# Performance work log

Measured on AMD Instinct MI355X. Metric: run time of the kernel, lower is better.

The kernel has to match this reference:

```python
import jax, jax.numpy as jnp
import numpy as np

B, S, D, H = 2, 2048, 1024, 16
DK = D // H

def setup_inputs() -> dict:
    key = jax.random.key(0)
    ks = jax.random.split(key, 8)
    scale = 1.0 / np.sqrt(D)
    return {
        "q": jax.random.normal(ks[0], (B, S, D), jnp.float32),
        "k": jax.random.normal(ks[1], (B, S, D), jnp.float32),
        "v": jax.random.normal(ks[2], (B, S, D), jnp.float32),
        "reaches": jax.random.uniform(ks[3], (B, S), jnp.float32),
        "Wq": jax.random.normal(ks[4], (D, D), jnp.float32) * scale,
        "Wk": jax.random.normal(ks[5], (D, D), jnp.float32) * scale,
        "Wv": jax.random.normal(ks[6], (D, D), jnp.float32) * scale,
        "Wo": jax.random.normal(ks[7], (D, D), jnp.float32) * scale,
    }

def _split_heads(x):
    # [B,S,D] -> [B,H,S,DK]
    return x.reshape(B, S, H, DK).transpose(0, 2, 1, 3)

def reference(q, k, v, reaches, Wq, Wk, Wv, Wo):
    # torch Linear: y = x @ W.T
    qh = _split_heads(q @ Wq.T)
    kh = _split_heads(k @ Wk.T)
    vh = _split_heads(v @ Wv.T)
    scores = jnp.einsum("bhqd,bhkd->bhqk", qh, kh) / jnp.sqrt(jnp.float32(DK))
    scores = jax.nn.softmax(scores, axis=-1)
    # post-softmax reach weighting along key axis
    scores = scores * reaches[:, None, None, :]
    # diagonal suppression: scores - scores*0.999999*eye
    scores = scores * (1.0 - 0.999999 * jnp.eye(S, dtype=scores.dtype))
    # inverted combine
    out = vh - jnp.einsum("bhqk,bhkd->bhqd", scores, vh)
    # per-position contribution rescale
    rs = reaches.sum(axis=-1, keepdims=True)
    contrib = (rs - reaches) / (rs + 1e-9) * (1.0 - reaches) * 100.0  # [B,S]
    out = out * contrib[:, None, :, None]
    concat = out.transpose(0, 2, 1, 3).reshape(B, S, D)
    return concat @ Wo.T
```

## Files before the change

kernel.cpp:

```cpp
#include <hip/hip_runtime.h>
#include <hip/hip_bf16.h>

typedef __attribute__((ext_vector_type(8))) short short8;
typedef __attribute__((ext_vector_type(4))) float f32x4;
typedef __attribute__((ext_vector_type(16))) float f32x16;
typedef unsigned short us;

#define B_ 2
#define S_ 2048
#define D_ 1024
#define H_ 16
#define DK_ 64
#define QSCALE 0.1803368867f

__device__ __forceinline__ us f2bf(float f) {
  union { float f; unsigned u; } x; x.f = f;
  unsigned r = x.u + 0x7FFFu + ((x.u >> 16) & 1u);
  return (us)(r >> 16);
}
__device__ __forceinline__ float bf2f(us h) {
  union { unsigned u; float f; } x; x.u = ((unsigned)h) << 16;
  return x.f;
}
__device__ __forceinline__ us f2bf_hw(float f) {
  __hip_bfloat16 h = __float2bfloat16(f);
  return *reinterpret_cast<us*>(&h);
}
__device__ __forceinline__ unsigned cvtpk(float lo, float hi) {
  unsigned r;
  asm("v_cvt_pk_bf16_f32 %0, %1, %2" : "=v"(r) : "v"(lo), "v"(hi));
  return r;
}

__device__ __forceinline__ void gload16(const void* g, void* l) {
  __builtin_amdgcn_global_load_lds((const __attribute__((address_space(1))) void*)g,
                                   (__attribute__((address_space(3))) void*)l, 16, 0, 0);
}

__global__ __launch_bounds__(256) void cvt_all(const float* __restrict__ q,
                                               const float* __restrict__ k,
                                               const float* __restrict__ v,
                                               const float* __restrict__ Wq,
                                               const float* __restrict__ Wk,
                                               const float* __restrict__ Wv,
                                               const float* __restrict__ Wo,
                                               us* __restrict__ oq, us* __restrict__ ok,
                                               us* __restrict__ ov, us* __restrict__ oWq,
                                               us* __restrict__ oWk, us* __restrict__ oWv,
                                               us* __restrict__ oWo) {
  int bid = blockIdx.x;
  const float* in; us* out; int off;
  if (bid < 12288) {
    int t = bid >> 12;
    in = (t == 0) ? q : (t == 1) ? k : v;
    out = (t == 0) ? oq : (t == 1) ? ok : ov;
    off = (bid & 4095) * 1024;
  } else {
    int t = (bid - 12288) >> 10;
    in = (t == 0) ? Wq : (t == 1) ? Wk : (t == 2) ? Wv : Wo;
    out = (t == 0) ? oWq : (t == 1) ? oWk : (t == 2) ? oWv : oWo;
    off = ((bid - 12288) & 1023) * 1024;
  }
  int i = off + threadIdx.x * 4;
  float4 val = *reinterpret_cast<const float4*>(in + i);
  ushort4 o;
  o.x = f2bf(val.x); o.y = f2bf(val.y); o.z = f2bf(val.z); o.w = f2bf(val.w);
  *reinterpret_cast<ushort4*>(out + i) = o;
}

__global__ __launch_bounds__(256) void rs_kernel(const float* __restrict__ reaches,
                                                 float* __restrict__ rs) {
  int b = blockIdx.x, t = threadIdx.x;
  float s = 0.f;
  for (int i = t; i < S_; i += 256) s += reaches[b * S_ + i];
  for (int o = 32; o > 0; o >>= 1) s += __shfl_down(s, o, 64);
  __shared__ float tmp[4];
  if ((t & 63) == 0) tmp[t >> 6] = s;
  __syncthreads();
  if (t == 0) rs[b] = tmp[0] + tmp[1] + tmp[2] + tmp[3];
}

__device__ __forceinline__ void gemm_core_hs(const us* __restrict__ A, const us* __restrict__ Bt,
                                             us* __restrict__ outH, float oscale) {
  __shared__ __align__(16) us lA[3][128 * 32];
  __shared__ __align__(16) us lB[3][128 * 32];
  const int tid = threadIdx.x;
  const int bm = blockIdx.x >> 3, bn = blockIdx.x & 7;
  const int w = tid >> 6, lane = tid & 63;
  const int wr = (w >> 1) * 64, wc = (w & 1) * 64;
  const int lr = lane & 15, lg = lane >> 4;

  f32x4 acc[4][4];
#pragma unroll
  for (int i = 0; i < 4; ++i)
#pragma unroll
    for (int j = 0; j < 4; ++j) acc[i][j] = (f32x4){0.f, 0.f, 0.f, 0.f};

  const int crow = lane >> 2, ce8 = (lane & 3) * 8;
  const us* A0 = A + (size_t)(bm * 128 + w * 32 + crow) * 1024 + ce8;
  const us* A1 = A0 + (size_t)16 * 1024;
  const us* B0 = Bt + (size_t)(bn * 128 + w * 32 + crow) * 1024 + ce8;
  const us* B1 = B0 + (size_t)16 * 1024;
  const int dA0 = (w * 32) * 32, dA1 = (w * 32 + 16) * 32;

  gload16(A0, &lA[0][dA0]);
  gload16(A1, &lA[0][dA1]);
  gload16(B0, &lB[0][dA0]);
  gload16(B1, &lB[0][dA1]);

  int cur = 0, nxt = 1;
  for (int kt = 0; kt < 32; ++kt) {
    if (kt < 31) {
      int ko = (kt + 1) * 32;
      gload16(A0 + ko, &lA[nxt][dA0]);
      gload16(A1 + ko, &lA[nxt][dA1]);
      gload16(B0 + ko, &lB[nxt][dA0]);
      gload16(B1 + ko, &lB[nxt][dA1]);
      asm volatile("s_waitcnt vmcnt(4)" ::: "memory");
    } else {
      asm volatile("s_waitcnt vmcnt(0)" ::: "memory");
    }
    __builtin_amdgcn_s_barrier();
    __builtin_amdgcn_sched_barrier(0);

    short8 af[4], bfr[4];
#pragma unroll
    for (int i = 0; i < 4; ++i)
      af[i] = *reinterpret_cast<const short8*>(&lA[cur][(wr + i * 16 + lr) * 32 + lg * 8]);
#pragma unroll
    for (int j = 0; j < 4; ++j)
      bfr[j] = *reinterpret_cast<const short8*>(&lB[cur][(wc + j * 16 + lr) * 32 + lg * 8]);
    __builtin_amdgcn_s_setprio(1);
#pragma unroll
    for (int i = 0; i < 4; ++i)
#pragma unroll
      for (int j = 0; j < 4; ++j)
        acc[i][j] = __builtin_amdgcn_mfma_f32_16x16x32_bf16(af[i], bfr[j], acc[i][j], 0, 0, 0);
    __builtin_amdgcn_s_setprio(0);

    cur = nxt;
    nxt = (nxt == 2) ? 0 : nxt + 1;
  }
#pragma unroll
  for (int i = 0; i < 4; ++i)
#pragma unroll
    for (int j = 0; j < 4; ++j)
#pragma unroll
      for (int ii = 0; ii < 4; ++ii) {
        int r = bm * 128 + wr + i * 16 + lg * 4 + ii;
        int c = bn * 128 + wc + j * 16 + lr;
        float v = acc[i][j][ii] * oscale;
        int b = r >> 11, s = r & (S_ - 1), h = c >> 6, dk = c & 63;
        outH[(((size_t)(b * H_ + h) * S_ + s) * DK_) + dk] = f2bf(v);
      }
}

__global__ __launch_bounds__(256) void proj_gemm(const us* __restrict__ q_bf,
                                                 const us* __restrict__ k_bf,
                                                 const us* __restrict__ v_bf,
                                                 const us* __restrict__ Wq_bf,
                                                 const us* __restrict__ Wk_bf,
                                                 const us* __restrict__ Wv_bf,
                                                 us* __restrict__ Qh, us* __restrict__ Kh,
                                                 us* __restrict__ Vh) {
  if (blockIdx.y == 0) gemm_core_hs(q_bf, Wq_bf, Qh, QSCALE);
  else if (blockIdx.y == 1) gemm_core_hs(k_bf, Wk_bf, Kh, 1.0f);
  else gemm_core_hs(v_bf, Wv_bf, Vh, 1.0f);
}

__global__ __launch_bounds__(256) void wo_gemm(const us* __restrict__ A,
                                               const us* __restrict__ Bt,
                                               float* __restrict__ outF) {
  __shared__ __align__(16) us lA[3][128 * 32];
  __shared__ __align__(16) us lB[3][64 * 32];
  const int tid = threadIdx.x;
  const int bm = blockIdx.x >> 4, bn = blockIdx.x & 15;
  const int w = tid >> 6, lane = tid & 63;
  const int lr = lane & 15, lg = lane >> 4;

  f32x4 acc[2][4];
#pragma unroll
  for (int i = 0; i < 2; ++i)
#pragma unroll
    for (int j = 0; j < 4; ++j) acc[i][j] = (f32x4){0.f, 0.f, 0.f, 0.f};

  const int crow = lane >> 2, ce8 = (lane & 3) * 8;
  const us* A0 = A + (size_t)(bm * 128 + w * 32 + crow) * 1024 + ce8;
  const us* A1 = A0 + (size_t)16 * 1024;
  const us* B0 = Bt + (size_t)(bn * 64 + w * 16 + crow) * 1024 + ce8;
  const int dA0 = (w * 32) * 32, dA1 = (w * 32 + 16) * 32, dB0 = (w * 16) * 32;

  gload16(A0, &lA[0][dA0]);
  gload16(A1, &lA[0][dA1]);
  gload16(B0, &lB[0][dB0]);

  int cur = 0, nxt = 1;
  for (int kt = 0; kt < 32; ++kt) {
    if (kt < 31) {
      int ko = (kt + 1) * 32;
      gload16(A0 + ko, &lA[nxt][dA0]);
      gload16(A1 + ko, &lA[nxt][dA1]);
      gload16(B0 + ko, &lB[nxt][dB0]);
      asm volatile("s_waitcnt vmcnt(3)" ::: "memory");
    } else {
      asm volatile("s_waitcnt vmcnt(0)" ::: "memory");
    }
    __builtin_amdgcn_s_barrier();
    __builtin_amdgcn_sched_barrier(0);

    short8 af[2], bfr[4];
#pragma unroll
    for (int i = 0; i < 2; ++i)
      af[i] = *reinterpret_cast<const short8*>(&lA[cur][(w * 32 + i * 16 + lr) * 32 + lg * 8]);
#pragma unroll
    for (int j = 0; j < 4; ++j)
      bfr[j] = *reinterpret_cast<const short8*>(&lB[cur][(j * 16 + lr) * 32 + lg * 8]);
    __builtin_amdgcn_s_setprio(1);
#pragma unroll
    for (int i = 0; i < 2; ++i)
#pragma unroll
      for (int j = 0; j < 4; ++j)
        acc[i][j] = __builtin_amdgcn_mfma_f32_16x16x32_bf16(af[i], bfr[j], acc[i][j], 0, 0, 0);
    __builtin_amdgcn_s_setprio(0);

    cur = nxt;
    nxt = (nxt == 2) ? 0 : nxt + 1;
  }
#pragma unroll
  for (int i = 0; i < 2; ++i)
#pragma unroll
    for (int j = 0; j < 4; ++j)
#pragma unroll
      for (int ii = 0; ii < 4; ++ii) {
        int r = bm * 128 + w * 32 + i * 16 + lg * 4 + ii;
        int c = bn * 64 + j * 16 + lr;
        outF[(size_t)r * 1024 + c] = acc[i][j][ii];
      }
}

__global__ __launch_bounds__(256) void transp_kernel(const us* __restrict__ Vh,
                                                     const float* __restrict__ reaches,
                                                     us* __restrict__ VhTw) {
  __shared__ us t[64 * 68];
  const int bh = blockIdx.x >> 5, st = blockIdx.x & 31;
  const int b = bh >> 4;
  const size_t base = (size_t)bh * S_ * DK_;
  const int r = threadIdx.x >> 3, e8 = (threadIdx.x & 7) * 8;
#pragma unroll
  for (int h2 = 0; h2 < 2; ++h2) {
    int row = r + h2 * 32;
    *reinterpret_cast<short8*>(&t[row * 68 + e8]) =
        *reinterpret_cast<const short8*>(&Vh[base + (size_t)(st * 64 + row) * DK_ + e8]);
  }
  __syncthreads();
#pragma unroll
  for (int h2 = 0; h2 < 2; ++h2) {
    int dk = (threadIdx.x >> 3) + h2 * 32;
    int sc = (threadIdx.x & 7) * 8;
    short8 v;
#pragma unroll
    for (int j = 0; j < 8; ++j) {
      float rw = reaches[b * S_ + st * 64 + sc + j];
      v[j] = (short)f2bf_hw(bf2f(t[(sc + j) * 68 + dk]) * rw);
    }
    *reinterpret_cast<short8*>(&VhTw[base + (size_t)dk * S_ + st * 64 + sc]) = v;
  }
}

__global__ __launch_bounds__(256, 2) void attn_kernel(const us* __restrict__ Qh,
                                                      const us* __restrict__ Kh,
                                                      const us* __restrict__ Vh,
                                                      const us* __restrict__ VhTw,
                                                      const float* __restrict__ reaches,
                                                      const float* __restrict__ rsum,
                                                      us* __restrict__ concat) {
  __shared__ __align__(16) us sbuf[3][8192];
  __shared__ float diagP[128];
  __shared__ float lsum[128];

  const int tid = threadIdx.x;
  const int bid = ((blockIdx.x & 7) << 6) | (blockIdx.x >> 3);
  const int qt = bid & 15;
  const int bh = bid >> 4;
  const int b = bh >> 4, h = bh & 15;
  const size_t base = (size_t)bh * S_ * DK_;

  const int w = tid >> 6, lane = tid & 63;
  const int l31 = lane & 31, hh = lane >> 5, l7 = lane & 7;
  const int h4 = hh * 4;
  const int diagkt = qt * 2 + (w >> 1);

  const int Lrow = lane >> 3;
  const int cswz = (l7 ^ Lrow) << 3;
  const us* Kg0 = Kh + base + (size_t)(w * 16 + Lrow) * DK_ + cswz;
  const us* Kg1 = Kg0 + (size_t)8 * DK_;
  const us* Vg0 = VhTw + base + (size_t)(w * 16 + Lrow) * S_ + cswz;
  const us* Vg1 = Vg0 + (size_t)8 * S_;
  const int dK0 = (w * 16) * 64, dK1 = (w * 16 + 8) * 64;
  const int dV0 = 4096 + dK0, dV1 = 4096 + dK1;

  short8 aq[4];
  {
    const us* qp = &Qh[base + (size_t)(qt * 128 + w * 32 + l31) * DK_ + hh * 8];
#pragma unroll
    for (int dk = 0; dk < 4; ++dk)
      aq[dk] = *reinterpret_cast<const short8*>(qp + dk * 16);
  }

  int rdK[2][4];
#pragma unroll
  for (int c = 0; c < 2; ++c)
#pragma unroll
    for (int dk = 0; dk < 4; ++dk)
      rdK[c][dk] = (c * 32 + l31) * 64 + (((dk * 2 + hh) ^ l7) << 3);

  gload16(Kg0, &sbuf[0][dK0]);
  gload16(Kg1, &sbuf[0][dK1]);
  gload16(Vg0, &sbuf[0][dV0]);
  gload16(Vg1, &sbuf[0][dV1]);

  f32x16 oacc[2];
  float lacc = 0.f;
#pragma unroll
  for (int c = 0; c < 2; ++c)
#pragma unroll
    for (int r = 0; r < 16; ++r) oacc[c][r] = 0.f;

  int cur = 0, nxt = 1;
  for (int kt = 0; kt < 32; ++kt) {
    if (kt < 31) {
      const size_t ko = (size_t)(kt + 1) * 64;
      gload16(Kg0 + ko * DK_, &sbuf[nxt][dK0]);
      gload16(Kg1 + ko * DK_, &sbuf[nxt][dK1]);
      gload16(Vg0 + ko, &sbuf[nxt][dV0]);
      gload16(Vg1 + ko, &sbuf[nxt][dV1]);
      asm volatile("s_waitcnt vmcnt(4)" ::: "memory");
    } else {
      asm volatile("s_waitcnt vmcnt(0)" ::: "memory");
    }
    __builtin_amdgcn_s_barrier();
    __builtin_amdgcn_sched_barrier(0);

    const us* lKc = &sbuf[cur][0];
    const us* vTc = &sbuf[cur][4096];

    f32x16 st0, st1;
#pragma unroll
    for (int r = 0; r < 16; ++r) { st0[r] = 0.f; st1[r] = 0.f; }
    __builtin_amdgcn_s_setprio(1);
#pragma unroll
    for (int dk = 0; dk < 4; ++dk) {
      short8 k0 = *reinterpret_cast<const short8*>(&lKc[rdK[0][dk]]);
      st0 = __builtin_amdgcn_mfma_f32_32x32x16_bf16(k0, aq[dk], st0, 0, 0, 0);
      short8 k1 = *reinterpret_cast<const short8*>(&lKc[rdK[1][dk]]);
      st1 = __builtin_amdgcn_mfma_f32_32x32x16_bf16(k1, aq[dk], st1, 0, 0, 0);
    }
    __builtin_amdgcn_s_setprio(0);

    float e0[16], e1[16];
#pragma unroll
    for (int r = 0; r < 16; ++r) {
      e0[r] = __builtin_amdgcn_exp2f(st0[r]);
      e1[r] = __builtin_amdgcn_exp2f(st1[r]);
      lacc += e0[r] + e1[r];
    }
    if (kt == diagkt) {
#pragma unroll
      for (int r = 0; r < 16; ++r) {
        int kk = (r & 3) + 8 * (r >> 2) + 4 * hh;
        float ev = (w & 1) ? e1[r] : e0[r];
        if (kk == l31) diagP[w * 32 + l31] = ev;
      }
    }

    short8 pa[4];
#pragma unroll
    for (int ks = 0; ks < 4; ++ks) {
      const int ro = (ks & 1) * 8;
      unsigned d0, s0, d1, s1;
      if (ks < 2) {
        d0 = cvtpk(e0[ro + 0], e0[ro + 1]);
        s0 = cvtpk(e0[ro + 4], e0[ro + 5]);
        d1 = cvtpk(e0[ro + 2], e0[ro + 3]);
        s1 = cvtpk(e0[ro + 6], e0[ro + 7]);
      } else {
        d0 = cvtpk(e1[ro + 0], e1[ro + 1]);
        s0 = cvtpk(e1[ro + 4], e1[ro + 5]);
        d1 = cvtpk(e1[ro + 2], e1[ro + 3]);
        s1 = cvtpk(e1[ro + 6], e1[ro + 7]);
      }
      asm("v_permlane32_swap_b32 %0, %1" : "+v"(d0), "+v"(s0));
      asm("v_permlane32_swap_b32 %0, %1" : "+v"(d1), "+v"(s1));
      union { unsigned u[4]; short8 v; } pk;
      pk.u[0] = d0; pk.u[1] = d1; pk.u[2] = s0; pk.u[3] = s1;
      pa[ks] = pk.v;
    }

    __builtin_amdgcn_s_setprio(1);
#pragma unroll
    for (int dc = 0; dc < 2; ++dc)
#pragma unroll
      for (int ks = 0; ks < 4; ++ks) {
        short8 bv = *reinterpret_cast<const short8*>(&vTc[rdK[dc][ks]]);
        oacc[dc] = __builtin_amdgcn_mfma_f32_32x32x16_bf16(pa[ks], bv, oacc[dc], 0, 0, 0);
      }
    __builtin_amdgcn_s_setprio(0);

    cur = nxt;
    nxt = (nxt == 2) ? 0 : nxt + 1;
  }

  lacc += __shfl_xor(lacc, 32, 64);
  if (hh == 0) lsum[w * 32 + l31] = lacc;
  __syncthreads();

  const float rb = rsum[b];
#pragma unroll
  for (int r = 0; r < 16; ++r) {
    const int q = w * 32 + (r & 3) + 8 * (r >> 2) + h4;
    const int qg = qt * 128 + q;
    const float rq = reaches[b * S_ + qg];
    const float contrib = (rb - rq) / (rb + 1e-9f) * (1.f - rq) * 100.f;
    const float corr = 0.999999f * diagP[q] * rq;
    const float linv = 1.0f / lsum[q];
#pragma unroll
    for (int dc = 0; dc < 2; ++dc) {
      int d = dc * 32 + l31;
      float vhv = bf2f(Vh[base + (size_t)qg * DK_ + d]);
      float pv = (oacc[dc][r] - corr * vhv) * linv;
      float o = (vhv - pv) * contrib;
      concat[((size_t)(b * S_ + qg)) * D_ + h * 64 + d] = f2bf(o);
    }
  }
}

extern "C" void kernel_launch(void* const* d_in, const int* in_sizes, int n_in,
                              void* d_out, int out_size, void* d_ws, size_t ws_size,
                              hipStream_t stream) {
  const float* q = (const float*)d_in[0];
  const float* k = (const float*)d_in[1];
  const float* v = (const float*)d_in[2];
  const float* reaches = (const float*)d_in[3];
  const float* Wq = (const float*)d_in[4];
  const float* Wk = (const float*)d_in[5];
  const float* Wv = (const float*)d_in[6];
  const float* Wo = (const float*)d_in[7];

  const size_t NQKV = (size_t)B_ * S_ * D_;
  const size_t NW = (size_t)D_ * D_;

  us* q_bf = (us*)d_ws;
  us* k_bf = q_bf + NQKV;
  us* v_bf = k_bf + NQKV;
  us* Wq_bf = v_bf + NQKV;
  us* Wk_bf = Wq_bf + NW;
  us* Wv_bf = Wk_bf + NW;
  us* Wo_bf = Wv_bf + NW;
  us* Qh = Wo_bf + NW;
  us* Kh = Qh + NQKV;
  us* Vh = Kh + NQKV;
  us* concat = Vh + NQKV;
  float* rs = (float*)(concat + NQKV);
  us* VhTw = q_bf;

  cvt_all<<<16384, 256, 0, stream>>>(q, k, v, Wq, Wk, Wv, Wo,
                                     q_bf, k_bf, v_bf, Wq_bf, Wk_bf, Wv_bf, Wo_bf);
  rs_kernel<<<B_, 256, 0, stream>>>(reaches, rs);

  proj_gemm<<<dim3(256, 3), 256, 0, stream>>>(q_bf, k_bf, v_bf, Wq_bf, Wk_bf, Wv_bf, Qh, Kh, Vh);
  transp_kernel<<<B_ * H_ * (S_ / 64), 256, 0, stream>>>(Vh, reaches, VhTw);

  attn_kernel<<<B_ * H_ * (S_ / 128), 256, 0, stream>>>(Qh, Kh, Vh, VhTw, reaches, rs, concat);

  wo_gemm<<<512, 256, 0, stream>>>(concat, Wo_bf, (float*)d_out);
}
```

Before: 133.2 us.

## Fold reach-sum into conversion kernel, swizzle GEMM tiles, register-staged attention loads

The reach-sum reduction now runs in one extra block of the conversion kernel, which removes a separate launch. The projection and output GEMMs remap block indices so that neighbouring blocks share operand tiles, aiming for better L2 reuse. The attention kernel replaces its triple-buffered direct global-to-LDS loads with register prefetch into a double-buffered LDS array, with a full block barrier each iteration. That change cuts LDS use, which may raise occupancy, but it adds register pressure and extra synchronisation, and global latency may be less well hidden.

After: 127.2 us (median of 3 runs). 1.05x faster.

```diff
diff --git a/kernel.cpp b/kernel.cpp
--- a/kernel.cpp
+++ b/kernel.cpp
@@ -44,11 +44,26 @@
                                                const float* __restrict__ Wk,
                                                const float* __restrict__ Wv,
                                                const float* __restrict__ Wo,
+                                               const float* __restrict__ reaches,
                                                us* __restrict__ oq, us* __restrict__ ok,
                                                us* __restrict__ ov, us* __restrict__ oWq,
                                                us* __restrict__ oWk, us* __restrict__ oWv,
-                                               us* __restrict__ oWo) {
+                                               us* __restrict__ oWo, float* __restrict__ rs) {
   int bid = blockIdx.x;
+  if (bid >= 16384) {
+    __shared__ float tmp[4];
+    int t = threadIdx.x;
+    for (int b = 0; b < B_; ++b) {
+      float s = 0.f;
+      for (int i = t; i < S_; i += 256) s += reaches[b * S_ + i];
+      for (int o = 32; o > 0; o >>= 1) s += __shfl_down(s, o, 64);
+      if ((t & 63) == 0) tmp[t >> 6] = s;
+      __syncthreads();
+      if (t == 0) rs[b] = tmp[0] + tmp[1] + tmp[2] + tmp[3];
+      __syncthreads();
+    }
+    return;
+  }
   const float* in; us* out; int off;
   if (bid < 12288) {
     int t = bid >> 12;
@@ -68,24 +83,13 @@
   *reinterpret_cast<ushort4*>(out + i) = o;
 }
 
-__global__ __launch_bounds__(256) void rs_kernel(const float* __restrict__ reaches,
-                                                 float* __restrict__ rs) {
-  int b = blockIdx.x, t = threadIdx.x;
-  float s = 0.f;
-  for (int i = t; i < S_; i += 256) s += reaches[b * S_ + i];
-  for (int o = 32; o > 0; o >>= 1) s += __shfl_down(s, o, 64);
-  __shared__ float tmp[4];
-  if ((t & 63) == 0) tmp[t >> 6] = s;
-  __syncthreads();
-  if (t == 0) rs[b] = tmp[0] + tmp[1] + tmp[2] + tmp[3];
-}
-
 __device__ __forceinline__ void gemm_core_hs(const us* __restrict__ A, const us* __restrict__ Bt,
                                              us* __restrict__ outH, float oscale) {
   __shared__ __align__(16) us lA[3][128 * 32];
   __shared__ __align__(16) us lB[3][128 * 32];
   const int tid = threadIdx.x;
-  const int bm = blockIdx.x >> 3, bn = blockIdx.x & 7;
+  const int swz = (blockIdx.x & 7) * 32 + (blockIdx.x >> 3);
+  const int bm = swz >> 3, bn = swz & 7;
   const int w = tid >> 6, lane = tid & 63;
   const int wr = (w >> 1) * 64, wc = (w & 1) * 64;
   const int lr = lane & 15, lg = lane >> 4;
@@ -174,7 +178,8 @@
   __shared__ __align__(16) us lA[3][128 * 32];
   __shared__ __align__(16) us lB[3][64 * 32];
   const int tid = threadIdx.x;
-  const int bm = blockIdx.x >> 4, bn = blockIdx.x & 15;
+  const int swz = (blockIdx.x & 7) * 64 + (blockIdx.x >> 3);
+  const int bm = swz >> 4, bn = swz & 15;
   const int w = tid >> 6, lane = tid & 63;
   const int lr = lane & 15, lg = lane >> 4;
 
@@ -274,7 +279,8 @@
                                                       const float* __restrict__ reaches,
                                                       const float* __restrict__ rsum,
                                                       us* __restrict__ concat) {
-  __shared__ __align__(16) us sbuf[3][8192];
+  __shared__ __align__(16) us lK2[2][64 * 64];
+  __shared__ __align__(16) us vT2[2][64 * 64];
   __shared__ float diagP[128];
   __shared__ float lsum[128];
 
@@ -288,16 +294,8 @@
   const int w = tid >> 6, lane = tid & 63;
   const int l31 = lane & 31, hh = lane >> 5, l7 = lane & 7;
   const int h4 = hh * 4;
+  const int r2 = tid >> 3, e8 = (tid & 7) * 8;
   const int diagkt = qt * 2 + (w >> 1);
-
-  const int Lrow = lane >> 3;
-  const int cswz = (l7 ^ Lrow) << 3;
-  const us* Kg0 = Kh + base + (size_t)(w * 16 + Lrow) * DK_ + cswz;
-  const us* Kg1 = Kg0 + (size_t)8 * DK_;
-  const us* Vg0 = VhTw + base + (size_t)(w * 16 + Lrow) * S_ + cswz;
-  const us* Vg1 = Vg0 + (size_t)8 * S_;
-  const int dK0 = (w * 16) * 64, dK1 = (w * 16 + 8) * 64;
-  const int dV0 = 4096 + dK0, dV1 = 4096 + dK1;
 
   short8 aq[4];
   {
@@ -313,11 +311,19 @@
 #pragma unroll
     for (int dk = 0; dk < 4; ++dk)
       rdK[c][dk] = (c * 32 + l31) * 64 + (((dk * 2 + hh) ^ l7) << 3);
-
-  gload16(Kg0, &sbuf[0][dK0]);
-  gload16(Kg1, &sbuf[0][dK1]);
-  gload16(Vg0, &sbuf[0][dV0]);
-  gload16(Vg1, &sbuf[0][dV1]);
+  const int wslot = ((tid & 7) ^ (r2 & 7)) << 3;
+  const int wK0 = r2 * 64 + wslot, wK1 = (r2 + 32) * 64 + wslot;
+
+  short8 pk0, pk1, pv0, pv1;
+  pk0 = *reinterpret_cast<const short8*>(&Kh[base + (size_t)r2 * DK_ + e8]);
+  pk1 = *reinterpret_cast<const short8*>(&Kh[base + (size_t)(r2 + 32) * DK_ + e8]);
+  pv0 = *reinterpret_cast<const short8*>(&VhTw[base + (size_t)r2 * S_ + e8]);
+  pv1 = *reinterpret_cast<const short8*>(&VhTw[base + (size_t)(r2 + 32) * S_ + e8]);
+  *reinterpret_cast<short8*>(&lK2[0][wK0]) = pk0;
+  *reinterpret_cast<short8*>(&lK2[0][wK1]) = pk1;
+  *reinterpret_cast<short8*>(&vT2[0][wK0]) = pv0;
+  *reinterpret_cast<short8*>(&vT2[0][wK1]) = pv1;
+  __syncthreads();
 
   f32x16 oacc[2];
   float lacc = 0.f;
@@ -326,23 +332,15 @@
 #pragma unroll
     for (int r = 0; r < 16; ++r) oacc[c][r] = 0.f;
 
-  int cur = 0, nxt = 1;
   for (int kt = 0; kt < 32; ++kt) {
+    const int cur = kt & 1;
     if (kt < 31) {
-      const size_t ko = (size_t)(kt + 1) * 64;
-      gload16(Kg0 + ko * DK_, &sbuf[nxt][dK0]);
-      gload16(Kg1 + ko * DK_, &sbuf[nxt][dK1]);
-      gload16(Vg0 + ko, &sbuf[nxt][dV0]);
-      gload16(Vg1 + ko, &sbuf[nxt][dV1]);
-      asm volatile("s_waitcnt vmcnt(4)" ::: "memory");
-    } else {
-      asm volatile("s_waitcnt vmcnt(0)" ::: "memory");
-    }
-    __builtin_amdgcn_s_barrier();
-    __builtin_amdgcn_sched_barrier(0);
-
-    const us* lKc = &sbuf[cur][0];
-    const us* vTc = &sbuf[cur][4096];
+      int nt = kt + 1;
+      pk0 = *reinterpret_cast<const short8*>(&Kh[base + (size_t)(nt * 64 + r2) * DK_ + e8]);
+      pk1 = *reinterpret_cast<const short8*>(&Kh[base + (size_t)(nt * 64 + r2 + 32) * DK_ + e8]);
+      pv0 = *reinterpret_cast<const short8*>(&VhTw[base + (size_t)r2 * S_ + nt * 64 + e8]);
+      pv1 = *reinterpret_cast<const short8*>(&VhTw[base + (size_t)(r2 + 32) * S_ + nt * 64 + e8]);
+    }
 
     f32x16 st0, st1;
 #pragma unroll
@@ -350,9 +348,9 @@
     __builtin_amdgcn_s_setprio(1);
 #pragma unroll
     for (int dk = 0; dk < 4; ++dk) {
-      short8 k0 = *reinterpret_cast<const short8*>(&lKc[rdK[0][dk]]);
+      short8 k0 = *reinterpret_cast<const short8*>(&lK2[cur][rdK[0][dk]]);
       st0 = __builtin_amdgcn_mfma_f32_32x32x16_bf16(k0, aq[dk], st0, 0, 0, 0);
-      short8 k1 = *reinterpret_cast<const short8*>(&lKc[rdK[1][dk]]);
+      short8 k1 = *reinterpret_cast<const short8*>(&lK2[cur][rdK[1][dk]]);
       st1 = __builtin_amdgcn_mfma_f32_32x32x16_bf16(k1, aq[dk], st1, 0, 0, 0);
     }
     __builtin_amdgcn_s_setprio(0);
@@ -401,13 +399,19 @@
     for (int dc = 0; dc < 2; ++dc)
 #pragma unroll
       for (int ks = 0; ks < 4; ++ks) {
-        short8 bv = *reinterpret_cast<const short8*>(&vTc[rdK[dc][ks]]);
+        short8 bv = *reinterpret_cast<const short8*>(&vT2[cur][rdK[dc][ks]]);
         oacc[dc] = __builtin_amdgcn_mfma_f32_32x32x16_bf16(pa[ks], bv, oacc[dc], 0, 0, 0);
       }
     __builtin_amdgcn_s_setprio(0);
 
-    cur = nxt;
-    nxt = (nxt == 2) ? 0 : nxt + 1;
+    if (kt < 31) {
+      const int nx = cur ^ 1;
+      *reinterpret_cast<short8*>(&lK2[nx][wK0]) = pk0;
+      *reinterpret_cast<short8*>(&lK2[nx][wK1]) = pk1;
+      *reinterpret_cast<short8*>(&vT2[nx][wK0]) = pv0;
+      *reinterpret_cast<short8*>(&vT2[nx][wK1]) = pv1;
+    }
+    __syncthreads();
   }
 
   lacc += __shfl_xor(lacc, 32, 64);
@@ -463,9 +467,8 @@
   float* rs = (float*)(concat + NQKV);
   us* VhTw = q_bf;
 
-  cvt_all<<<16384, 256, 0, stream>>>(q, k, v, Wq, Wk, Wv, Wo,
-                                     q_bf, k_bf, v_bf, Wq_bf, Wk_bf, Wv_bf, Wo_bf);
-  rs_kernel<<<B_, 256, 0, stream>>>(reaches, rs);
+  cvt_all<<<16385, 256, 0, stream>>>(q, k, v, Wq, Wk, Wv, Wo, reaches,
+                                     q_bf, k_bf, v_bf, Wq_bf, Wk_bf, Wv_bf, Wo_bf, rs);
 
   proj_gemm<<<dim3(256, 3), 256, 0, stream>>>(q_bf, k_bf, v_bf, Wq_bf, Wk_bf, Wv_bf, Qh, Kh, Vh);
   transp_kernel<<<B_ * H_ * (S_ / 64), 256, 0, stream>>>(Vh, reaches, VhTw);
```
